# Performance work log

Measured on AMD Instinct MI355X. Metric: run time of the kernel, lower is better.

The kernel has to match this reference:

```python
import jax, jax.numpy as jnp
import numpy as np

K, D = 8, 32          # num_heads, node_out_dim
KD = K * D            # 256
NEG = 0.2             # LeakyReLU negative slope
N, E = 100000, 300000
DIN, DREL = 128, 64


def setup_inputs() -> dict:
    key = jax.random.key(0)
    ks = iter(jax.random.split(key, 64))
    def nrm(shape, scale):
        return jax.random.normal(next(ks), shape, jnp.float32) * scale
    inp = {}
    # per-relation target-node features feats[(s,e,d)] : (N_d, d_in)
    for nm in ["feat_ui", "feat_iu", "feat_ii", "feat_ii_rev"]:
        inp[nm] = nrm((N, DIN), 1.0)
    # relation input features (d_rel,)
    for nm in ["r_ui", "r_iu", "r_ii", "r_ii_rev"]:
        inp[nm] = nrm((DREL,), 1.0)
    # fc_node per ntype (no bias), shared for src/dst roles
    inp["W_user"] = nrm((DIN, KD), 0.05)
    inp["W_item"] = nrm((DIN, KD), 0.05)
    # fc_rel per etype (no bias): d_rel -> 2*K*d
    for nm in ["Wrel_ui", "Wrel_iu", "Wrel_ii", "Wrel_ii_rev"]:
        inp[nm] = nrm((DREL, 2 * KD), 0.05)
    # cross-relation attention vectors (K, d)
    for nm in ["attn_ui", "attn_iu", "attn_ii", "attn_ii_rev"]:
        inp[nm] = nrm((K, D), 0.1)
    # residual fc per ntype (with bias) and residual gate scalar
    inp["Wres_user"] = nrm((DIN, KD), 0.05); inp["bres_user"] = nrm((KD,), 0.02)
    inp["Wres_item"] = nrm((DIN, KD), 0.05); inp["bres_item"] = nrm((KD,), 0.02)
    inp["a_user"] = jax.random.uniform(next(ks), (1,), jnp.float32)
    inp["a_item"] = jax.random.uniform(next(ks), (1,), jnp.float32)
    # fc_upd per etype (with bias): d_rel -> K*rel_out
    for nm in ["ui", "iu", "ii", "ii_rev"]:
        inp["Wupd_" + nm] = nrm((DREL, KD), 0.05)
        inp["bupd_" + nm] = nrm((KD,), 0.02)
    # edge lists per relation
    for nm in ["ui", "iu", "ii", "ii_rev"]:
        inp["src_" + nm] = jax.random.randint(next(ks), (E,), 0, N, jnp.int32)
        inp["dst_" + nm] = jax.random.randint(next(ks), (E,), 0, N, jnp.int32)
    return inp


def _conv(fsrc_in, fdst_in, Ws, Wd, Wrel, rfeat, src, dst):
    """RelationGraphConv: GAT-style attention over one bipartite relation."""
    n_dst = fdst_in.shape[0]
    fs = (fsrc_in @ Ws).reshape(-1, K, D)          # (Ns, K, D)
    fd = (fdst_in @ Wd).reshape(-1, K, D)          # (Nd, K, D)
    attn = (rfeat @ Wrel).reshape(K, 2 * D)        # (K, 2D)
    el = (fs * attn[:, :D]).sum(-1)                # (Ns, K)
    er = (fd * attn[:, D:]).sum(-1)                # (Nd, K)
    e = jax.nn.leaky_relu(el[src] + er[dst], NEG)  # (E, K)
    # edge softmax per destination node
    m = jax.ops.segment_max(e, dst, num_segments=n_dst)
    ex = jnp.exp(e - m[dst])
    s = jax.ops.segment_sum(ex, dst, num_segments=n_dst)
    a = ex / s[dst]                                # (E, K)
    msg = fs[src] * a[:, :, None]                  # (E, K, D)
    out = jax.ops.segment_sum(msg, dst, num_segments=n_dst)
    return jax.nn.relu(out.reshape(n_dst, KD))     # activation = relu


def _crossing(stacked, rel_attn):
    """RelationCrossing over stacked per-relation dst reps (R, N, K*D)."""
    R, Nn = stacked.shape[0], stacked.shape[1]
    f = stacked.reshape(R, Nn, K, D)
    sc = (rel_attn * f).sum(-1, keepdims=True)             # (R, N, K, 1)
    sc = jax.nn.softmax(jax.nn.leaky_relu(sc, NEG), axis=0)
    return (sc * f).sum(0).reshape(Nn, KD)


def reference(feat_ui, feat_iu, feat_ii, feat_ii_rev,
              r_ui, r_iu, r_ii, r_ii_rev,
              W_user, W_item,
              Wrel_ui, Wrel_iu, Wrel_ii, Wrel_ii_rev,
              attn_ui, attn_iu, attn_ii, attn_ii_rev,
              Wres_user, bres_user, Wres_item, bres_item,
              a_user, a_item,
              Wupd_ui, bupd_ui, Wupd_iu, bupd_iu,
              Wupd_ii, bupd_ii, Wupd_ii_rev, bupd_ii_rev,
              src_ui, dst_ui, src_iu, dst_iu,
              src_ii, dst_ii, src_ii_rev, dst_ii_rev):
    # relation convs; src feats come from the reverse relation's dict entry
    h_ui = _conv(feat_iu, feat_ui, W_user, W_item, Wrel_ui, r_ui, src_ui, dst_ui)
    h_iu = _conv(feat_ui, feat_iu, W_item, W_user, Wrel_iu, r_iu, src_iu, dst_iu)
    h_ii = _conv(feat_ii_rev, feat_ii, W_item, W_item, Wrel_ii, r_ii, src_ii, dst_ii)
    h_iir = _conv(feat_ii, feat_ii_rev, W_item, W_item, Wrel_ii_rev, r_ii_rev, src_ii_rev, dst_ii_rev)

    # gated residual per dtype
    def resid(h, fdst, Wres, bres, a):
        al = jax.nn.sigmoid(a)
        return al * h + (1.0 - al) * (fdst @ Wres + bres)

    h_ui = resid(h_ui, feat_ui, Wres_item, bres_item, a_item)
    h_iu = resid(h_iu, feat_iu, Wres_user, bres_user, a_user)
    h_ii = resid(h_ii, feat_ii, Wres_item, bres_item, a_item)
    h_iir = resid(h_iir, feat_ii_rev, Wres_item, bres_item, a_item)

    # cross-relation fusion: dtype item has relations [ui, ii, ii_rev]; user has [iu]
    item_stack = jnp.stack([h_ui, h_ii, h_iir], axis=0)
    out_ui = _crossing(item_stack, attn_ui)
    out_iu = h_iu  # num_rel == 1 -> identity
    out_ii = _crossing(item_stack, attn_ii)
    out_iir = _crossing(item_stack, attn_ii_rev)

    # relation feature update
    ro_ui = r_ui @ Wupd_ui + bupd_ui
    ro_iu = r_iu @ Wupd_iu + bupd_iu
    ro_ii = r_ii @ Wupd_ii + bupd_ii
    ro_iir = r_ii_rev @ Wupd_ii_rev + bupd_ii_rev
    return (out_ui, out_iu, out_ii, out_iir, ro_ui, ro_iu, ro_ii, ro_iir)
```

## Files before the change

### kernel.cpp

```cpp
#include <hip/hip_runtime.h>
#include <hip/hip_bf16.h>
#include <math.h>

#define NEG_SLOPE 0.2f
#define LOG2E 1.4426950408889634f

using bf16x8 = __attribute__((ext_vector_type(8))) short;
using f32x4  = __attribute__((ext_vector_type(4))) float;
using u16x8  = __attribute__((ext_vector_type(8))) unsigned short;
using u16x4  = __attribute__((ext_vector_type(4))) unsigned short;

__device__ __forceinline__ float lrelu(float x) { return x > 0.f ? x : NEG_SLOPE * x; }
__device__ __forceinline__ float dot4(float4 a, float4 b) {
    return a.x * b.x + a.y * b.y + a.z * b.z + a.w * b.w;
}
__device__ __forceinline__ unsigned short f2b(float x) {
    union { float f; unsigned u; } v; v.f = x;
    unsigned r = v.u + 0x7fff + ((v.u >> 16) & 1);
    return (unsigned short)(r >> 16);
}
__device__ __forceinline__ float b2f(unsigned short b) {
    union { unsigned u; float f; } v; v.u = ((unsigned)b) << 16;
    return v.f;
}
__device__ __forceinline__ float4 load4b(const unsigned short* p) {
    u16x4 u = *reinterpret_cast<const u16x4*>(p);
    return make_float4(b2f(u[0]), b2f(u[1]), b2f(u[2]), b2f(u[3]));
}

struct PackArgs {
    const float* W1[2];
    const float* W2[2];
    unsigned short* Bp[2];
};

__global__ __launch_bounds__(256)
void pack_b_k(PackArgs pa)
{
    const int p = blockIdx.y;
    const int gid = blockIdx.x * 256 + threadIdx.x;
    const int lane = gid & 63;
    const int grp = gid >> 6;
    const int ks = grp & 3;
    const int nb = grp >> 2;
    const int n = nb * 16 + (lane & 15);
    const int k0 = ks * 32 + (lane >> 4) * 8;
    const float* Wsrc = (n < 256) ? (pa.W1[p] + n) : (pa.W2[p] + (n - 256));
    u16x8 u;
    #pragma unroll
    for (int e = 0; e < 8; ++e) u[e] = f2b(Wsrc[(size_t)(k0 + e) * 256]);
    *reinterpret_cast<u16x8*>(pa.Bp[p] + (size_t)gid * 8) = u;
}

struct GemmArgs {
    const float* A[4];
    const unsigned short* Bp[4];
    const float* bres[4];
    unsigned short* pool[4];
    unsigned short* resid[4];
    const float* wvA[4];
    const float* wvB[4];
    float* elOut[4];
    float* erOut[4];
};

__global__ __launch_bounds__(512)
void mfma_gemm_k(GemmArgs ga, int Nrows)
{
    __shared__ __align__(16) char smem[65536];
    unsigned short* Asw = (unsigned short*)smem;
    const int rsel = blockIdx.y;
    const float* __restrict__ A = ga.A[rsel];
    const unsigned short* __restrict__ Bp = ga.Bp[rsel];
    const float* __restrict__ bres = ga.bres[rsel];
    const int t = threadIdx.x;
    const int m0 = blockIdx.x * 128;

    #pragma unroll
    for (int i = 0; i < 4; ++i) {
        const int idx = i * 512 + t;
        const int row = idx >> 4;
        const int cg  = idx & 15;
        float4 a0 = make_float4(0.f, 0.f, 0.f, 0.f), a1 = a0;
        if (m0 + row < Nrows) {
            const float* p = A + (size_t)(m0 + row) * 128 + cg * 8;
            a0 = *reinterpret_cast<const float4*>(p);
            a1 = *reinterpret_cast<const float4*>(p + 4);
        }
        u16x8 u;
        u[0] = f2b(a0.x); u[1] = f2b(a0.y); u[2] = f2b(a0.z); u[3] = f2b(a0.w);
        u[4] = f2b(a1.x); u[5] = f2b(a1.y); u[6] = f2b(a1.z); u[7] = f2b(a1.w);
        const int off = row * 256 + ((cg * 16) ^ ((row & 7) << 4));
        *reinterpret_cast<u16x8*>((char*)Asw + off) = u;
    }
    __syncthreads();

    const int wv = t >> 6, lane = t & 63;
    const int mh = wv >> 2;
    const int wn = wv & 3;
    const int l15 = lane & 15, lg = lane >> 4;
    const int nbb = wn * 8;

    f32x4 acc[4][8];
    #pragma unroll
    for (int mi = 0; mi < 4; ++mi)
        #pragma unroll
        for (int ni = 0; ni < 8; ++ni)
            acc[mi][ni] = (f32x4){0.f, 0.f, 0.f, 0.f};

    #pragma unroll
    for (int ks = 0; ks < 4; ++ks) {
        bf16x8 bfr[8];
        #pragma unroll
        for (int ni = 0; ni < 8; ++ni)
            bfr[ni] = *reinterpret_cast<const bf16x8*>(
                Bp + (size_t)(((nbb + ni) * 4 + ks) * 64 + lane) * 8);
        bf16x8 afr[4];
        #pragma unroll
        for (int mi = 0; mi < 4; ++mi) {
            const int row = mh * 64 + mi * 16 + l15;
            const int off = row * 256 + ((ks * 64 + lg * 16) ^ ((row & 7) << 4));
            afr[mi] = *reinterpret_cast<const bf16x8*>((const char*)Asw + off);
        }
        #pragma unroll
        for (int mi = 0; mi < 4; ++mi)
            #pragma unroll
            for (int ni = 0; ni < 8; ++ni)
                acc[mi][ni] = __builtin_amdgcn_mfma_f32_16x16x32_bf16(
                    afr[mi], bfr[ni], acc[mi][ni], 0, 0, 0);
    }
    __syncthreads();

    if (wn < 2) {
        const int colbase = wn * 128;
        #pragma unroll
        for (int ni = 0; ni < 8; ++ni) {
            const int col = colbase + ni * 16 + l15;
            #pragma unroll
            for (int mi = 0; mi < 4; ++mi) {
                #pragma unroll
                for (int r = 0; r < 4; ++r) {
                    const int row = mh * 64 + mi * 16 + lg * 4 + r;
                    const int byte = row * 512 + ((col * 2) ^ ((row & 7) << 4));
                    *reinterpret_cast<unsigned short*>(smem + byte) =
                        f2b(acc[mi][ni][r]);
                }
            }
        }
    }
    __syncthreads();
    {
        unsigned short* dst = ga.pool[rsel];
        #pragma unroll
        for (int i = 0; i < 8; ++i) {
            const int idx = i * 512 + t;
            const int row = idx >> 5;
            const int c16 = idx & 31;
            const int byte = row * 512 + ((c16 * 16) ^ ((row & 7) << 4));
            u16x8 v = *reinterpret_cast<const u16x8*>(smem + byte);
            if (m0 + row < Nrows)
                *reinterpret_cast<u16x8*>(dst + (size_t)(m0 + row) * 256 + c16 * 8) = v;
        }
    }
    #pragma unroll
    for (int q = 0; q < 2; ++q) {
        const int task = q * 512 + t;
        const int ro = task >> 3, kk = task & 7;
        float pl = 0.f, pr = 0.f;
        const float* __restrict__ wA = ga.wvA[rsel] + kk * 64;
        const float* __restrict__ wB = ga.wvB[rsel] + kk * 64 + 32;
        #pragma unroll
        for (int j2 = 0; j2 < 4; ++j2) {
            const int col = kk * 32 + j2 * 8;
            const int byte = ro * 512 + ((col * 2) ^ ((ro & 7) << 4));
            u16x8 u = *reinterpret_cast<const u16x8*>(smem + byte);
            #pragma unroll
            for (int e = 0; e < 8; ++e) {
                const float v = b2f(u[e]);
                pl = fmaf(v, wA[j2 * 8 + e], pl);
                pr = fmaf(v, wB[j2 * 8 + e], pr);
            }
        }
        if (m0 + ro < Nrows) {
            ga.elOut[rsel][(size_t)(m0 + ro) * 8 + kk] = pl;
            ga.erOut[rsel][(size_t)(m0 + ro) * 8 + kk] = pr;
        }
    }
    __syncthreads();

    if (wn >= 2) {
        const int colbase = (wn & 1) * 128;
        #pragma unroll
        for (int ni = 0; ni < 8; ++ni) {
            const int col = colbase + ni * 16 + l15;
            const float bv = bres[col];
            #pragma unroll
            for (int mi = 0; mi < 4; ++mi) {
                #pragma unroll
                for (int r = 0; r < 4; ++r) {
                    const int row = mh * 64 + mi * 16 + lg * 4 + r;
                    const int byte = row * 512 + ((col * 2) ^ ((row & 7) << 4));
                    *reinterpret_cast<unsigned short*>(smem + byte) =
                        f2b(acc[mi][ni][r] + bv);
                }
            }
        }
    }
    __syncthreads();
    {
        unsigned short* dst = ga.resid[rsel];
        #pragma unroll
        for (int i = 0; i < 8; ++i) {
            const int idx = i * 512 + t;
            const int row = idx >> 5;
            const int c16 = idx & 31;
            const int byte = row * 512 + ((c16 * 16) ^ ((row & 7) << 4));
            u16x8 v = *reinterpret_cast<const u16x8*>(smem + byte);
            if (m0 + row < Nrows)
                *reinterpret_cast<u16x8*>(dst + (size_t)(m0 + row) * 256 + c16 * 8) = v;
        }
    }
}

struct EdgePtrs {
    const int* src[4];
    const int* dst[4];
    int E[4];
    int csrOff[4];
};

__global__ __launch_bounds__(256)
void hist_k(EdgePtrs ep, int* __restrict__ counts4, int N)
{
    const int r = blockIdx.y;
    const int e = blockIdx.x * 256 + threadIdx.x;
    if (e < ep.E[r]) atomicAdd(counts4 + (size_t)r * N + ep.dst[r][e], 1);
}

__global__ __launch_bounds__(256)
void blksum_k(const int* __restrict__ counts4, int* __restrict__ blksum4, int N)
{
    const int r = blockIdx.y;
    const int* c = counts4 + (size_t)r * N;
    const int base = blockIdx.x * 1024 + threadIdx.x;
    int s = 0;
    #pragma unroll
    for (int i = 0; i < 4; ++i) { int idx = base + i * 256; if (idx < N) s += c[idx]; }
    __shared__ int sd[256];
    sd[threadIdx.x] = s; __syncthreads();
    for (int off = 128; off > 0; off >>= 1) {
        if (threadIdx.x < off) sd[threadIdx.x] += sd[threadIdx.x + off];
        __syncthreads();
    }
    if (threadIdx.x == 0) blksum4[r * 1024 + blockIdx.x] = sd[0];
}

__global__ __launch_bounds__(1024)
void scanblk_k(int* __restrict__ blksum4, int nbx)
{
    const int r = blockIdx.x;
    const int t = threadIdx.x;
    __shared__ int sd[1024];
    int v = (t < nbx) ? blksum4[r * 1024 + t] : 0;
    sd[t] = v; __syncthreads();
    for (int off = 1; off < 1024; off <<= 1) {
        int u = (t >= off) ? sd[t - off] : 0;
        __syncthreads();
        sd[t] += u;
        __syncthreads();
    }
    if (t < nbx) blksum4[r * 1024 + t] = sd[t] - v;
}

__global__ __launch_bounds__(256)
void cursor_k(const int* __restrict__ counts4, const int* __restrict__ blkoff4,
              int* __restrict__ cursor4, int N)
{
    const int r = blockIdx.y;
    const int* c = counts4 + (size_t)r * N;
    int* cur = cursor4 + (size_t)r * N;
    const int t = threadIdx.x;
    const int base = blockIdx.x * 1024 + t * 4;
    const int c0 = (base + 0 < N) ? c[base + 0] : 0;
    const int c1 = (base + 1 < N) ? c[base + 1] : 0;
    const int c2 = (base + 2 < N) ? c[base + 2] : 0;
    const int c3 = (base + 3 < N) ? c[base + 3] : 0;
    const int tsum = c0 + c1 + c2 + c3;
    __shared__ int sd[256];
    sd[t] = tsum; __syncthreads();
    for (int off = 1; off < 256; off <<= 1) {
        int u = (t >= off) ? sd[t - off] : 0;
        __syncthreads();
        sd[t] += u;
        __syncthreads();
    }
    int excl = sd[t] - tsum + blkoff4[r * 1024 + blockIdx.x];
    if (base + 0 < N) cur[base + 0] = excl;
    if (base + 1 < N) cur[base + 1] = excl + c0;
    if (base + 2 < N) cur[base + 2] = excl + c0 + c1;
    if (base + 3 < N) cur[base + 3] = excl + c0 + c1 + c2;
}

__global__ __launch_bounds__(256)
void scatter_k(EdgePtrs ep, int* __restrict__ cursor4, int* __restrict__ csr_src, int N)
{
    const int r = blockIdx.y;
    const int e = blockIdx.x * 256 + threadIdx.x;
    if (e < ep.E[r]) {
        const int d = ep.dst[r][e];
        const int pos = atomicAdd(cursor4 + (size_t)r * N + d, 1);
        csr_src[ep.csrOff[r] + pos] = ep.src[r][e];
    }
}

struct NodeArgs {
    const int* csr[4];
    const int* cursor[4];
    const int* counts[4];
    const float* el[4];
    const float* er[4];
    const unsigned short* pool[4];
    const unsigned short* resid[4];
};

__global__ __launch_bounds__(256)
void node_k(NodeArgs na,
            const float* __restrict__ attn_ui, const float* __restrict__ attn_ii,
            const float* __restrict__ attn_iir,
            const float* __restrict__ a_user, const float* __restrict__ a_item,
            float* __restrict__ out, int Nrows)
{
    const int lane = threadIdx.x & 63;
    const int n = blockIdx.x * 4 + (threadIdx.x >> 6);
    if (n >= Nrows) return;
    const int k = lane >> 3;

    int deg[4], endv[4];
    float erk[4];
    #pragma unroll
    for (int r = 0; r < 4; ++r) {
        deg[r]  = na.counts[r][n];
        endv[r] = na.cursor[r][n];
        erk[r]  = na.er[r][(size_t)n * 8 + k];
    }

    const float si = 1.f / (1.f + __expf(-a_item[0])), osi = 1.f - si;
    const float su = 1.f / (1.f + __expf(-a_user[0])), osu = 1.f - su;

    float4 fr[4];
    #pragma unroll
    for (int r = 0; r < 4; ++r) {
        const int d = deg[r];
        const int start = endv[r] - d;
        const int* __restrict__ csr = na.csr[r];
        const float* __restrict__ elr = na.el[r];
        const unsigned short* __restrict__ fs = na.pool[r];
        const float er_k = erk[r];
        float s = 0.f;
        float4 acc = make_float4(0.f, 0.f, 0.f, 0.f);
        for (int base = 0; base < d; base += 4) {
            const int m = d - base;
            int sidx[4];
            #pragma unroll
            for (int u = 0; u < 4; ++u)
                sidx[u] = csr[start + base + ((u < m) ? u : 0)];
            float ex[4];
            #pragma unroll
            for (int u = 0; u < 4; ++u) {
                const float x = elr[(size_t)sidx[u] * 8 + k] + er_k;
                const float e = __builtin_amdgcn_exp2f(fmaxf(x, NEG_SLOPE * x));
                ex[u] = (u < m) ? e : 0.f;
            }
            float4 pv[4];
            #pragma unroll
            for (int u = 0; u < 4; ++u)
                pv[u] = load4b(fs + (size_t)sidx[u] * 256 + lane * 4);
            #pragma unroll
            for (int u = 0; u < 4; ++u) {
                s += ex[u];
                acc.x = fmaf(pv[u].x, ex[u], acc.x);
                acc.y = fmaf(pv[u].y, ex[u], acc.y);
                acc.z = fmaf(pv[u].z, ex[u], acc.z);
                acc.w = fmaf(pv[u].w, ex[u], acc.w);
            }
        }
        const float inv = (d > 0) ? 1.f / s : 0.f;
        float4 R = load4b(na.resid[r] + (size_t)n * 256 + lane * 4);
        const float sg = (r == 1) ? su : si;
        const float og = (r == 1) ? osu : osi;
        fr[r].x = sg * fmaxf(acc.x * inv, 0.f) + og * R.x;
        fr[r].y = sg * fmaxf(acc.y * inv, 0.f) + og * R.y;
        fr[r].z = sg * fmaxf(acc.z * inv, 0.f) + og * R.z;
        fr[r].w = sg * fmaxf(acc.w * inv, 0.f) + og * R.w;
    }

    const float4 f0 = fr[0], f1 = fr[2], f2 = fr[3], fiu = fr[1];
    float4 w0 = *reinterpret_cast<const float4*>(attn_ui  + lane * 4);
    float4 w1 = *reinterpret_cast<const float4*>(attn_ii  + lane * 4);
    float4 w2 = *reinterpret_cast<const float4*>(attn_iir + lane * 4);

    float p[3][3];
    p[0][0] = dot4(w0, f0); p[0][1] = dot4(w0, f1); p[0][2] = dot4(w0, f2);
    p[1][0] = dot4(w1, f0); p[1][1] = dot4(w1, f1); p[1][2] = dot4(w1, f2);
    p[2][0] = dot4(w2, f0); p[2][1] = dot4(w2, f1); p[2][2] = dot4(w2, f2);
    #pragma unroll
    for (int x = 0; x < 3; ++x)
        #pragma unroll
        for (int r = 0; r < 3; ++r)
            #pragma unroll
            for (int m = 1; m < 8; m <<= 1)
                p[x][r] += __shfl_xor(p[x][r], m, 64);

    const size_t NK = (size_t)Nrows * 256;
    const size_t o = (size_t)n * 256 + lane * 4;
    const size_t xoff[3] = {0, 2 * NK, 3 * NK};
    #pragma unroll
    for (int x = 0; x < 3; ++x) {
        float a0 = lrelu(p[x][0]), a1 = lrelu(p[x][1]), a2 = lrelu(p[x][2]);
        float mx = fmaxf(a0, fmaxf(a1, a2));
        float e0 = __expf(a0 - mx), e1 = __expf(a1 - mx), e2 = __expf(a2 - mx);
        float inv = 1.f / (e0 + e1 + e2);
        e0 *= inv; e1 *= inv; e2 *= inv;
        float4 rr;
        rr.x = e0 * f0.x + e1 * f1.x + e2 * f2.x;
        rr.y = e0 * f0.y + e1 * f1.y + e2 * f2.y;
        rr.z = e0 * f0.z + e1 * f1.z + e2 * f2.z;
        rr.w = e0 * f0.w + e1 * f1.w + e2 * f2.w;
        *reinterpret_cast<float4*>(out + xoff[x] + o) = rr;
    }
    *reinterpret_cast<float4*>(out + NK + o) = fiu;
}

struct RelPtrs {
    const float* rf[4];
    const float* Wrel[4];
    const float* Wupd[4];
    const float* bupd[4];
};

__global__ __launch_bounds__(512)
void rel_k(RelPtrs P, float* __restrict__ wvec, float* __restrict__ ro)
{
    const int r = blockIdx.x;
    const int t = threadIdx.x;
    __shared__ float rfs[64];
    if (t < 64) rfs[t] = P.rf[r][t];
    __syncthreads();
    {
        const float* Wc = P.Wrel[r];
        float acc = 0.f;
        #pragma unroll 8
        for (int i = 0; i < 64; ++i) acc = fmaf(rfs[i], Wc[(size_t)i * 512 + t], acc);
        wvec[(size_t)r * 512 + t] = acc * LOG2E;
    }
    if (t < 256) {
        const float* Wc = P.Wupd[r];
        float acc = P.bupd[r][t];
        #pragma unroll 8
        for (int i = 0; i < 64; ++i) acc = fmaf(rfs[i], Wc[(size_t)i * 256 + t], acc);
        ro[(size_t)r * 256 + t] = acc;
    }
}

extern "C" void kernel_launch(void* const* d_in, const int* in_sizes, int n_in,
                              void* d_out, int out_size, void* d_ws, size_t ws_size,
                              hipStream_t stream)
{
    (void)n_in; (void)out_size; (void)ws_size;
    const float* feat_ui  = (const float*)d_in[0];
    const float* feat_iu  = (const float*)d_in[1];
    const float* feat_ii  = (const float*)d_in[2];
    const float* feat_iir = (const float*)d_in[3];
    const float* W_user   = (const float*)d_in[8];
    const float* W_item   = (const float*)d_in[9];
    const float* Wres_user = (const float*)d_in[18];
    const float* bres_user = (const float*)d_in[19];
    const float* Wres_item = (const float*)d_in[20];
    const float* bres_item = (const float*)d_in[21];
    const float* a_user = (const float*)d_in[22];
    const float* a_item = (const float*)d_in[23];
    const int N = in_sizes[0] / 128;
    const int Es[4] = {in_sizes[32], in_sizes[34], in_sizes[36], in_sizes[38]};
    int maxE = 0;
    for (int r = 0; r < 4; ++r) maxE = Es[r] > maxE ? Es[r] : maxE;

    const size_t NP = (size_t)N * 256;
    const size_t N8 = (size_t)N * 8;

    unsigned short* us = (unsigned short*)d_ws;
    unsigned short* pool[4];
    unsigned short* resid[4];
    for (int r = 0; r < 4; ++r) pool[r]  = us + (size_t)r * NP;
    for (int r = 0; r < 4; ++r) resid[r] = us + (size_t)(4 + r) * NP;
    unsigned short* Bp_user = us + 8 * NP;
    unsigned short* Bp_item = Bp_user + 65536;
    float* fl = (float*)(Bp_item + 65536);
    float *el[4], *er[4];
    for (int r = 0; r < 4; ++r) { el[r] = fl + (size_t)(2 * r) * N8; er[r] = fl + (size_t)(2 * r + 1) * N8; }
    float* wvec = fl + 8 * N8;
    int* counts4 = (int*)(wvec + 4 * 512);
    int* cursor4 = counts4 + 4 * (size_t)N;
    int* blksum4 = cursor4 + 4 * (size_t)N;
    int* csr_src = blksum4 + 4 * 1024;
    float* out = (float*)d_out;

    EdgePtrs ep;
    {
        int off = 0;
        const int si[4] = {32, 34, 36, 38};
        for (int r = 0; r < 4; ++r) {
            ep.src[r] = (const int*)d_in[si[r]];
            ep.dst[r] = (const int*)d_in[si[r] + 1];
            ep.E[r] = Es[r];
            ep.csrOff[r] = off;
            off += Es[r];
        }
    }

    (void)hipMemsetAsync(counts4, 0, 4 * (size_t)N * sizeof(int), stream);

    RelPtrs rp;
    rp.rf[0]   = (const float*)d_in[4];  rp.rf[1]   = (const float*)d_in[5];
    rp.rf[2]   = (const float*)d_in[6];  rp.rf[3]   = (const float*)d_in[7];
    rp.Wrel[0] = (const float*)d_in[10]; rp.Wrel[1] = (const float*)d_in[11];
    rp.Wrel[2] = (const float*)d_in[12]; rp.Wrel[3] = (const float*)d_in[13];
    rp.Wupd[0] = (const float*)d_in[24]; rp.Wupd[1] = (const float*)d_in[26];
    rp.Wupd[2] = (const float*)d_in[28]; rp.Wupd[3] = (const float*)d_in[30];
    rp.bupd[0] = (const float*)d_in[25]; rp.bupd[1] = (const float*)d_in[27];
    rp.bupd[2] = (const float*)d_in[29]; rp.bupd[3] = (const float*)d_in[31];
    rel_k<<<dim3(4), dim3(512), 0, stream>>>(rp, wvec, out + 4 * NP);

    PackArgs pa;
    pa.W1[0] = W_user; pa.W2[0] = Wres_user; pa.Bp[0] = Bp_user;
    pa.W1[1] = W_item; pa.W2[1] = Wres_item; pa.Bp[1] = Bp_item;
    pack_b_k<<<dim3(32, 2), 256, 0, stream>>>(pa);

    const int geb = (maxE + 255) / 256;
    const int nbx = (N + 1023) / 1024;
    hist_k<<<dim3(geb, 4), 256, 0, stream>>>(ep, counts4, N);
    blksum_k<<<dim3(nbx, 4), 256, 0, stream>>>(counts4, blksum4, N);
    scanblk_k<<<dim3(4), 1024, 0, stream>>>(blksum4, nbx);
    cursor_k<<<dim3(nbx, 4), 256, 0, stream>>>(counts4, blksum4, cursor4, N);
    scatter_k<<<dim3(geb, 4), 256, 0, stream>>>(ep, cursor4, csr_src, N);

    const int pair[4] = {1, 0, 3, 2};
    GemmArgs ga;
    ga.A[0] = feat_iu;  ga.Bp[0] = Bp_user; ga.bres[0] = bres_user; ga.pool[0] = pool[0]; ga.resid[0] = resid[1];
    ga.A[1] = feat_ui;  ga.Bp[1] = Bp_item; ga.bres[1] = bres_item; ga.pool[1] = pool[1]; ga.resid[1] = resid[0];
    ga.A[2] = feat_iir; ga.Bp[2] = Bp_item; ga.bres[2] = bres_item; ga.pool[2] = pool[2]; ga.resid[2] = resid[3];
    ga.A[3] = feat_ii;  ga.Bp[3] = Bp_item; ga.bres[3] = bres_item; ga.pool[3] = pool[3]; ga.resid[3] = resid[2];
    for (int r = 0; r < 4; ++r) {
        ga.wvA[r]   = wvec + (size_t)r * 512;
        ga.wvB[r]   = wvec + (size_t)pair[r] * 512;
        ga.elOut[r] = el[r];
        ga.erOut[r] = er[pair[r]];
    }
    const int gb = (N + 127) / 128;
    mfma_gemm_k<<<dim3(gb, 4), 512, 0, stream>>>(ga, N);

    NodeArgs na;
    for (int r = 0; r < 4; ++r) {
        na.csr[r]    = csr_src + ep.csrOff[r];
        na.cursor[r] = cursor4 + (size_t)r * N;
        na.counts[r] = counts4 + (size_t)r * N;
        na.el[r]     = el[r];
        na.er[r]     = er[r];
        na.pool[r]   = pool[r];
        na.resid[r]  = resid[r];
    }
    const int nb4 = (N + 3) / 4;
    node_k<<<nb4, 256, 0, stream>>>(na,
                                    (const float*)d_in[14], (const float*)d_in[16],
                                    (const float*)d_in[17],
                                    a_user, a_item, out, N);
}
```

Measured before the change: 688.5 us.

## Fold attention projections into GEMM weights and drop LDS staging in node GEMM

Precomputes W·attn columns for el/er during weight packing, so the attention logits come out of the same MFMA GEMM as extra output columns instead of a separate LDS-based reduction. The GEMM kernel is restructured so each wave handles 16 nodes with A held in registers. It loops over 33 column tiles, streams packed B from global/cache, and writes pool, residual and el/er directly without shared memory or block barriers. This removes LDS traffic and syncs, at the cost of re-reading B per wave, smaller-width stores, and slightly different rounding for el/er (bf16 folded weights).

```diff
diff --git a/kernel.cpp b/kernel.cpp
--- a/kernel.cpp
+++ b/kernel.cpp
@@ -27,29 +27,51 @@
     u16x4 u = *reinterpret_cast<const u16x4*>(p);
     return make_float4(b2f(u[0]), b2f(u[1]), b2f(u[2]), b2f(u[3]));
 }
+__device__ __forceinline__ bf16x8 cvt8(float4 a0, float4 a1) {
+    union { u16x8 u; bf16x8 b; } c;
+    c.u[0] = f2b(a0.x); c.u[1] = f2b(a0.y); c.u[2] = f2b(a0.z); c.u[3] = f2b(a0.w);
+    c.u[4] = f2b(a1.x); c.u[5] = f2b(a1.y); c.u[6] = f2b(a1.z); c.u[7] = f2b(a1.w);
+    return c.b;
+}
 
 struct PackArgs {
-    const float* W1[2];
-    const float* W2[2];
-    unsigned short* Bp[2];
+    const float* W1[4];
+    const float* W2[4];
+    const float* wvA[4];
+    const float* wvB[4];
+    unsigned short* Bp[4];
 };
 
 __global__ __launch_bounds__(256)
 void pack_b_k(PackArgs pa)
 {
-    const int p = blockIdx.y;
-    const int gid = blockIdx.x * 256 + threadIdx.x;
-    const int lane = gid & 63;
-    const int grp = gid >> 6;
-    const int ks = grp & 3;
-    const int nb = grp >> 2;
+    const int r = blockIdx.y;
+    const int nb = blockIdx.x;
+    const int ks = threadIdx.x >> 6;
+    const int lane = threadIdx.x & 63;
     const int n = nb * 16 + (lane & 15);
     const int k0 = ks * 32 + (lane >> 4) * 8;
-    const float* Wsrc = (n < 256) ? (pa.W1[p] + n) : (pa.W2[p] + (n - 256));
     u16x8 u;
-    #pragma unroll
-    for (int e = 0; e < 8; ++e) u[e] = f2b(Wsrc[(size_t)(k0 + e) * 256]);
-    *reinterpret_cast<u16x8*>(pa.Bp[p] + (size_t)gid * 8) = u;
+    if (n < 512) {
+        const float* Wsrc = (n < 256) ? (pa.W1[r] + n) : (pa.W2[r] + (n - 256));
+        #pragma unroll
+        for (int e = 0; e < 8; ++e) u[e] = f2b(Wsrc[(size_t)(k0 + e) * 256]);
+    } else {
+        const int h = (n - 512) & 7;
+        const bool isEr = (n >= 520);
+        const float* wv = isEr ? (pa.wvB[r] + h * 64 + 32) : (pa.wvA[r] + h * 64);
+        const float* Wc = pa.W1[r] + h * 32;
+        #pragma unroll
+        for (int e = 0; e < 8; ++e) {
+            const size_t k = (size_t)(k0 + e);
+            float s = 0.f;
+            #pragma unroll 8
+            for (int d = 0; d < 32; ++d) s = fmaf(Wc[k * 256 + d], wv[d], s);
+            u[e] = f2b(s);
+        }
+    }
+    const size_t gid = (size_t)((nb * 4 + ks) * 64 + lane);
+    *reinterpret_cast<u16x8*>(pa.Bp[r] + gid * 8) = u;
 }
 
 struct GemmArgs {
@@ -58,166 +80,67 @@
     const float* bres[4];
     unsigned short* pool[4];
     unsigned short* resid[4];
-    const float* wvA[4];
-    const float* wvB[4];
     float* elOut[4];
     float* erOut[4];
 };
 
-__global__ __launch_bounds__(512)
+__global__ __launch_bounds__(256)
 void mfma_gemm_k(GemmArgs ga, int Nrows)
 {
-    __shared__ __align__(16) char smem[65536];
-    unsigned short* Asw = (unsigned short*)smem;
     const int rsel = blockIdx.y;
+    const int t = threadIdx.x;
+    const int wv = t >> 6, lane = t & 63;
+    const int l15 = lane & 15, lg = lane >> 4;
+    const int node = blockIdx.x * 64 + wv * 16 + l15;
+    const bool valid = node < Nrows;
+    const int nc = valid ? node : (Nrows - 1);
+
     const float* __restrict__ A = ga.A[rsel];
     const unsigned short* __restrict__ Bp = ga.Bp[rsel];
     const float* __restrict__ bres = ga.bres[rsel];
-    const int t = threadIdx.x;
-    const int m0 = blockIdx.x * 128;
-
-    #pragma unroll
-    for (int i = 0; i < 4; ++i) {
-        const int idx = i * 512 + t;
-        const int row = idx >> 4;
-        const int cg  = idx & 15;
-        float4 a0 = make_float4(0.f, 0.f, 0.f, 0.f), a1 = a0;
-        if (m0 + row < Nrows) {
-            const float* p = A + (size_t)(m0 + row) * 128 + cg * 8;
-            a0 = *reinterpret_cast<const float4*>(p);
-            a1 = *reinterpret_cast<const float4*>(p + 4);
+    unsigned short* __restrict__ poolp = ga.pool[rsel];
+    unsigned short* __restrict__ resp  = ga.resid[rsel];
+
+    bf16x8 bfr[4];
+    #pragma unroll
+    for (int ks = 0; ks < 4; ++ks) {
+        const float* p = A + (size_t)nc * 128 + ks * 32 + lg * 8;
+        float4 a0 = *reinterpret_cast<const float4*>(p);
+        float4 a1 = *reinterpret_cast<const float4*>(p + 4);
+        bfr[ks] = cvt8(a0, a1);
+    }
+
+    #pragma unroll
+    for (int ni = 0; ni < 33; ++ni) {
+        f32x4 acc = (f32x4){0.f, 0.f, 0.f, 0.f};
+        #pragma unroll
+        for (int ks = 0; ks < 4; ++ks) {
+            bf16x8 wf = *reinterpret_cast<const bf16x8*>(
+                Bp + ((size_t)((ni * 4 + ks) * 64 + lane)) * 8);
+            acc = __builtin_amdgcn_mfma_f32_16x16x32_bf16(wf, bfr[ks], acc, 0, 0, 0);
         }
-        u16x8 u;
-        u[0] = f2b(a0.x); u[1] = f2b(a0.y); u[2] = f2b(a0.z); u[3] = f2b(a0.w);
-        u[4] = f2b(a1.x); u[5] = f2b(a1.y); u[6] = f2b(a1.z); u[7] = f2b(a1.w);
-        const int off = row * 256 + ((cg * 16) ^ ((row & 7) << 4));
-        *reinterpret_cast<u16x8*>((char*)Asw + off) = u;
-    }
-    __syncthreads();
-
-    const int wv = t >> 6, lane = t & 63;
-    const int mh = wv >> 2;
-    const int wn = wv & 3;
-    const int l15 = lane & 15, lg = lane >> 4;
-    const int nbb = wn * 8;
-
-    f32x4 acc[4][8];
-    #pragma unroll
-    for (int mi = 0; mi < 4; ++mi)
-        #pragma unroll
-        for (int ni = 0; ni < 8; ++ni)
-            acc[mi][ni] = (f32x4){0.f, 0.f, 0.f, 0.f};
-
-    #pragma unroll
-    for (int ks = 0; ks < 4; ++ks) {
-        bf16x8 bfr[8];
-        #pragma unroll
-        for (int ni = 0; ni < 8; ++ni)
-            bfr[ni] = *reinterpret_cast<const bf16x8*>(
-                Bp + (size_t)(((nbb + ni) * 4 + ks) * 64 + lane) * 8);
-        bf16x8 afr[4];
-        #pragma unroll
-        for (int mi = 0; mi < 4; ++mi) {
-            const int row = mh * 64 + mi * 16 + l15;
-            const int off = row * 256 + ((ks * 64 + lg * 16) ^ ((row & 7) << 4));
-            afr[mi] = *reinterpret_cast<const bf16x8*>((const char*)Asw + off);
-        }
-        #pragma unroll
-        for (int mi = 0; mi < 4; ++mi)
-            #pragma unroll
-            for (int ni = 0; ni < 8; ++ni)
-                acc[mi][ni] = __builtin_amdgcn_mfma_f32_16x16x32_bf16(
-                    afr[mi], bfr[ni], acc[mi][ni], 0, 0, 0);
-    }
-    __syncthreads();
-
-    if (wn < 2) {
-        const int colbase = wn * 128;
-        #pragma unroll
-        for (int ni = 0; ni < 8; ++ni) {
-            const int col = colbase + ni * 16 + l15;
-            #pragma unroll
-            for (int mi = 0; mi < 4; ++mi) {
-                #pragma unroll
-                for (int r = 0; r < 4; ++r) {
-                    const int row = mh * 64 + mi * 16 + lg * 4 + r;
-                    const int byte = row * 512 + ((col * 2) ^ ((row & 7) << 4));
-                    *reinterpret_cast<unsigned short*>(smem + byte) =
-                        f2b(acc[mi][ni][r]);
-                }
+        if (ni < 16) {
+            if (valid) {
+                u16x4 o;
+                o[0] = f2b(acc[0]); o[1] = f2b(acc[1]);
+                o[2] = f2b(acc[2]); o[3] = f2b(acc[3]);
+                *reinterpret_cast<u16x4*>(poolp + (size_t)node * 256 + ni * 16 + lg * 4) = o;
             }
-        }
-    }
-    __syncthreads();
-    {
-        unsigned short* dst = ga.pool[rsel];
-        #pragma unroll
-        for (int i = 0; i < 8; ++i) {
-            const int idx = i * 512 + t;
-            const int row = idx >> 5;
-            const int c16 = idx & 31;
-            const int byte = row * 512 + ((c16 * 16) ^ ((row & 7) << 4));
-            u16x8 v = *reinterpret_cast<const u16x8*>(smem + byte);
-            if (m0 + row < Nrows)
-                *reinterpret_cast<u16x8*>(dst + (size_t)(m0 + row) * 256 + c16 * 8) = v;
-        }
-    }
-    #pragma unroll
-    for (int q = 0; q < 2; ++q) {
-        const int task = q * 512 + t;
-        const int ro = task >> 3, kk = task & 7;
-        float pl = 0.f, pr = 0.f;
-        const float* __restrict__ wA = ga.wvA[rsel] + kk * 64;
-        const float* __restrict__ wB = ga.wvB[rsel] + kk * 64 + 32;
-        #pragma unroll
-        for (int j2 = 0; j2 < 4; ++j2) {
-            const int col = kk * 32 + j2 * 8;
-            const int byte = ro * 512 + ((col * 2) ^ ((ro & 7) << 4));
-            u16x8 u = *reinterpret_cast<const u16x8*>(smem + byte);
-            #pragma unroll
-            for (int e = 0; e < 8; ++e) {
-                const float v = b2f(u[e]);
-                pl = fmaf(v, wA[j2 * 8 + e], pl);
-                pr = fmaf(v, wB[j2 * 8 + e], pr);
+        } else if (ni < 32) {
+            const int cb = (ni - 16) * 16 + lg * 4;
+            float4 bv = *reinterpret_cast<const float4*>(bres + cb);
+            if (valid) {
+                u16x4 o;
+                o[0] = f2b(acc[0] + bv.x); o[1] = f2b(acc[1] + bv.y);
+                o[2] = f2b(acc[2] + bv.z); o[3] = f2b(acc[3] + bv.w);
+                *reinterpret_cast<u16x4*>(resp + (size_t)node * 256 + cb) = o;
             }
-        }
-        if (m0 + ro < Nrows) {
-            ga.elOut[rsel][(size_t)(m0 + ro) * 8 + kk] = pl;
-            ga.erOut[rsel][(size_t)(m0 + ro) * 8 + kk] = pr;
-        }
-    }
-    __syncthreads();
-
-    if (wn >= 2) {
-        const int colbase = (wn & 1) * 128;
-        #pragma unroll
-        for (int ni = 0; ni < 8; ++ni) {
-            const int col = colbase + ni * 16 + l15;
-            const float bv = bres[col];
-            #pragma unroll
-            for (int mi = 0; mi < 4; ++mi) {
-                #pragma unroll
-                for (int r = 0; r < 4; ++r) {
-                    const int row = mh * 64 + mi * 16 + lg * 4 + r;
-                    const int byte = row * 512 + ((col * 2) ^ ((row & 7) << 4));
-                    *reinterpret_cast<unsigned short*>(smem + byte) =
-                        f2b(acc[mi][ni][r] + bv);
-                }
-            }
-        }
-    }
-    __syncthreads();
-    {
-        unsigned short* dst = ga.resid[rsel];
-        #pragma unroll
-        for (int i = 0; i < 8; ++i) {
-            const int idx = i * 512 + t;
-            const int row = idx >> 5;
-            const int c16 = idx & 31;
-            const int byte = row * 512 + ((c16 * 16) ^ ((row & 7) << 4));
-            u16x8 v = *reinterpret_cast<const u16x8*>(smem + byte);
-            if (m0 + row < Nrows)
-                *reinterpret_cast<u16x8*>(dst + (size_t)(m0 + row) * 256 + c16 * 8) = v;
+        } else if (valid) {
+            float4 v = make_float4(acc[0], acc[1], acc[2], acc[3]);
+            if (lg < 2)
+                *reinterpret_cast<float4*>(ga.elOut[rsel] + (size_t)node * 8 + lg * 4) = v;
+            else
+                *reinterpret_cast<float4*>(ga.erOut[rsel] + (size_t)node * 8 + (lg - 2) * 4) = v;
         }
     }
 }
@@ -486,15 +409,16 @@
 
     const size_t NP = (size_t)N * 256;
     const size_t N8 = (size_t)N * 8;
+    const size_t BPSZ = 33 * 4 * 64 * 8;
 
     unsigned short* us = (unsigned short*)d_ws;
     unsigned short* pool[4];
     unsigned short* resid[4];
     for (int r = 0; r < 4; ++r) pool[r]  = us + (size_t)r * NP;
     for (int r = 0; r < 4; ++r) resid[r] = us + (size_t)(4 + r) * NP;
-    unsigned short* Bp_user = us + 8 * NP;
-    unsigned short* Bp_item = Bp_user + 65536;
-    float* fl = (float*)(Bp_item + 65536);
+    unsigned short* BpArr[4];
+    for (int r = 0; r < 4; ++r) BpArr[r] = us + 8 * NP + (size_t)r * BPSZ;
+    float* fl = (float*)(us + 8 * NP + 4 * BPSZ);
     float *el[4], *er[4];
     for (int r = 0; r < 4; ++r) { el[r] = fl + (size_t)(2 * r) * N8; er[r] = fl + (size_t)(2 * r + 1) * N8; }
     float* wvec = fl + 8 * N8;
@@ -530,10 +454,18 @@
     rp.bupd[2] = (const float*)d_in[29]; rp.bupd[3] = (const float*)d_in[31];
     rel_k<<<dim3(4), dim3(512), 0, stream>>>(rp, wvec, out + 4 * NP);
 
+    const int pair[4] = {1, 0, 3, 2};
     PackArgs pa;
-    pa.W1[0] = W_user; pa.W2[0] = Wres_user; pa.Bp[0] = Bp_user;
-    pa.W1[1] = W_item; pa.W2[1] = Wres_item; pa.Bp[1] = Bp_item;
-    pack_b_k<<<dim3(32, 2), 256, 0, stream>>>(pa);
+    pa.W1[0] = W_user; pa.W2[0] = Wres_user;
+    pa.W1[1] = W_item; pa.W2[1] = Wres_item;
+    pa.W1[2] = W_item; pa.W2[2] = Wres_item;
+    pa.W1[3] = W_item; pa.W2[3] = Wres_item;
+    for (int r = 0; r < 4; ++r) {
+        pa.wvA[r] = wvec + (size_t)r * 512;
+        pa.wvB[r] = wvec + (size_t)pair[r] * 512;
+        pa.Bp[r]  = BpArr[r];
+    }
+    pack_b_k<<<dim3(33, 4), 256, 0, stream>>>(pa);
 
     const int geb = (maxE + 255) / 256;
     const int nbx = (N + 1023) / 1024;
@@ -543,20 +475,20 @@
     cursor_k<<<dim3(nbx, 4), 256, 0, stream>>>(counts4, blksum4, cursor4, N);
     scatter_k<<<dim3(geb, 4), 256, 0, stream>>>(ep, cursor4, csr_src, N);
 
-    const int pair[4] = {1, 0, 3, 2};
     GemmArgs ga;
-    ga.A[0] = feat_iu;  ga.Bp[0] = Bp_user; ga.bres[0] = bres_user; ga.pool[0] = pool[0]; ga.resid[0] = resid[1];
-    ga.A[1] = feat_ui;  ga.Bp[1] = Bp_item; ga.bres[1] = bres_item; ga.pool[1] = pool[1]; ga.resid[1] = resid[0];
-    ga.A[2] = feat_iir; ga.Bp[2] = Bp_item; ga.bres[2] = bres_item; ga.pool[2] = pool[2]; ga.resid[2] = resid[3];
-    ga.A[3] = feat_ii;  ga.Bp[3] = Bp_item; ga.bres[3] = bres_item; ga.pool[3] = pool[3]; ga.resid[3] = resid[2];
+    ga.A[0] = feat_iu;  ga.bres[0] = bres_user;
+    ga.A[1] = feat_ui;  ga.bres[1] = bres_item;
+    ga.A[2] = feat_iir; ga.bres[2] = bres_item;
+    ga.A[3] = feat_ii;  ga.bres[3] = bres_item;
     for (int r = 0; r < 4; ++r) {
-        ga.wvA[r]   = wvec + (size_t)r * 512;
-        ga.wvB[r]   = wvec + (size_t)pair[r] * 512;
+        ga.Bp[r]    = BpArr[r];
+        ga.pool[r]  = pool[r];
+        ga.resid[r] = resid[pair[r]];
         ga.elOut[r] = el[r];
         ga.erOut[r] = er[pair[r]];
     }
-    const int gb = (N + 127) / 128;
-    mfma_gemm_k<<<dim3(gb, 4), 512, 0, stream>>>(ga, N);
+    const int gb = (N + 63) / 64;
+    mfma_gemm_k<<<dim3(gb, 4), 256, 0, stream>>>(ga, N);
 
     NodeArgs na;
     for (int r = 0; r < 4; ++r) {
```

Measured after the change: 726.8 us. 5.6% more time.
